# Optimization experiments

Hardware: AMD Instinct MI355X
Metric: run time of the kernel (lower is better)

Reference implementation:

```python
import jax, jax.numpy as jnp
from jax import lax
import numpy as np

B, C, O, NF, H, W = 4, 64, 64, 64, 128, 128
DK = 3
K = DK * DK
PAD = DK // 2


def setup_inputs() -> dict:
    key = jax.random.key(0)
    k0, k1, k2, k3 = jax.random.split(key, 4)
    inputs = jax.random.normal(k0, (B, C, H, W), jnp.float32)
    feat = jax.random.normal(k1, (B, NF, H, W), jnp.float32)
    # small offset-conv weights keep learned offsets in a realistic sub-pixel range
    om_w = jax.random.normal(k2, (C * 3 * K, NF, 3, 3), jnp.float32) * 0.02
    om_b = jnp.zeros((C * 3 * K,), jnp.float32)
    dc_w = jax.random.normal(k3, (O, C, DK, DK), jnp.float32) * (1.0 / np.sqrt(C * K))
    dc_b = jnp.zeros((O,), jnp.float32)
    return dict(inputs=inputs, feat=feat, om_w=om_w, om_b=om_b, dc_w=dc_w, dc_b=dc_b)


def _gather(img, y, x):
    # img: [B,C,H,W]; y,x: int32 [B,C,K,H,W]; zero outside bounds
    valid = (y >= 0) & (y < H) & (x >= 0) & (x < W)
    yc = jnp.clip(y, 0, H - 1)
    xc = jnp.clip(x, 0, W - 1)
    idx = (yc * W + xc).reshape(B, C, K, H * W)
    flat = img.reshape(B, C, 1, H * W)
    v = jnp.take_along_axis(flat, idx, axis=3).reshape(B, C, K, H, W)
    return jnp.where(valid, v, 0.0)


def _forward(inputs, feat, om_w, om_b, dc_w, dc_b):
    # offset/mask conv: nf -> in_nc*3*K, 3x3, pad 1
    off_msk = lax.conv_general_dilated(
        feat, om_w, (1, 1), ((1, 1), (1, 1)),
        dimension_numbers=('NCHW', 'OIHW', 'NCHW')) + om_b[None, :, None, None]
    # offsets interleaved (y,x) per kernel tap per deformable group (= channel)
    off = off_msk[:, :C * 2 * K].reshape(B, C, K, 2, H, W)
    msk = jax.nn.sigmoid(off_msk[:, C * 2 * K:]).reshape(B, C, K, H, W)

    ky = (jnp.arange(K) // DK - PAD).astype(jnp.float32)  # [K]
    kx = (jnp.arange(K) % DK - PAD).astype(jnp.float32)
    hg = jnp.arange(H, dtype=jnp.float32)
    wg = jnp.arange(W, dtype=jnp.float32)
    py = hg[None, None, None, :, None] + ky[None, None, :, None, None] + off[:, :, :, 0]  # [B,C,K,H,W]
    px = wg[None, None, None, None, :] + kx[None, None, :, None, None] + off[:, :, :, 1]

    y0f = jnp.floor(py); x0f = jnp.floor(px)
    wy = py - y0f; wx = px - x0f
    y0 = y0f.astype(jnp.int32); x0 = x0f.astype(jnp.int32)
    y1 = y0 + 1; x1 = x0 + 1

    v00 = _gather(inputs, y0, x0)
    v01 = _gather(inputs, y0, x1)
    v10 = _gather(inputs, y1, x0)
    v11 = _gather(inputs, y1, x1)
    sampled = ((1 - wy) * (1 - wx) * v00 + (1 - wy) * wx * v01
               + wy * (1 - wx) * v10 + wy * wx * v11) * msk  # [B,C,K,H,W]

    out = jnp.einsum('bckhw,ock->bohw', sampled, dc_w.reshape(O, C, K))
    out = out + dc_b[None, :, None, None]
    return jax.nn.relu(out)


def reference(inputs, feat, om_w, om_b, dc_w, dc_b):
    return _forward(inputs, feat, om_w, om_b, dc_w, dc_b)
```

## Files before the change

kernel.cpp:

```cpp
#include <hip/hip_runtime.h>
#include <hip/hip_bf16.h>

typedef __bf16 bf16;
typedef __bf16 bf16x8 __attribute__((ext_vector_type(8)));
typedef __bf16 bf16x4 __attribute__((ext_vector_type(4)));
typedef float f32x4 __attribute__((ext_vector_type(4)));

#define MFMA16(a, b, c) __builtin_amdgcn_mfma_f32_16x16x32_bf16((a), (b), (c), 0, 0, 0)

static constexpr size_t FEAT_OFF = 0;
static constexpr size_t OMW3_OFF = 8388608;
static constexpr size_t OMB_OFF  = OMW3_OFF + 1990656;
static constexpr size_t DCW_OFF  = OMB_OFF + 6912;
static constexpr size_t PAD_OFF  = DCW_OFF + 73728;

__global__ void prep_cvt(const float* __restrict__ in, bf16* __restrict__ out, int n) {
    int i = blockIdx.x * 256 + threadIdx.x;
    if (i < n) out[i] = (bf16)in[i];
}

__global__ void prep_omw3(const float* __restrict__ om_w, bf16* __restrict__ out) {
    int i = blockIdx.x * 256 + threadIdx.x;
    if (i >= 995328) return;
    int e = i & 511, lane = e >> 3, j = e & 7;
    int q = i >> 9;
    int t = q % 3, q2 = q / 3, kk = q2 % 18, ct = q2 / 18;
    int ck = ct * 16 + (lane & 15);
    int kcol = kk * 32 + (lane >> 4) * 8 + j;
    int tap = kcol >> 6, cf = kcol & 63;
    int ch = (t < 2) ? (ck * 2 + t) : (1152 + ck);
    out[i] = (bf16)om_w[ch * 576 + cf * 9 + tap];
}

__global__ void prep_dcw2p(const float* __restrict__ dc_w, const float* __restrict__ om_b,
                           bf16* __restrict__ dcw2p, float* __restrict__ ombr) {
    int i = blockIdx.x * 256 + threadIdx.x;
    if (i < 36864) {
        int j = i & 7, lane = (i >> 3) & 63, ot = (i >> 9) & 3, win = i >> 11;
        int o = ot * 16 + (lane & 15);
        int ck = win * 32 + (lane >> 4) * 8 + j;
        dcw2p[i] = (bf16)dc_w[o * 576 + ck];
    }
    if (i < 1728) {
        int t = i / 576, ck = i - t * 576;
        int ch = (t < 2) ? (ck * 2 + t) : (1152 + ck);
        ombr[i] = om_b[ch];
    }
}

__global__ void prep_pad(const float* __restrict__ inputs, float* __restrict__ pad) {
    int yy = blockIdx.x, bc = blockIdx.y, xx = threadIdx.x;
    if (xx >= 134) return;
    float v = 0.f;
    if (yy >= 3 && yy <= 130 && xx >= 3 && xx <= 130)
        v = inputs[(size_t)bc * 16384 + (yy - 3) * 128 + (xx - 3)];
    pad[((size_t)bc * 134 + yy) * 134 + xx] = v;
}


__global__ void __launch_bounds__(256) __attribute__((amdgpu_waves_per_eu(2, 2)))
deform_fused(const float* __restrict__ pad,
             const bf16* __restrict__ featbf,
             const bf16* __restrict__ omw3,
             const float* __restrict__ ombr,
             const bf16* __restrict__ dcw2p,
             const float* __restrict__ dcb,
             float* __restrict__ out)
{
    const int bh = blockIdx.x;
    const int b = bh >> 7, h = bh & 127;
    const int tid = threadIdx.x;
    const int lane = tid & 63, wid = tid >> 6;
    const int l15 = lane & 15, g = lane >> 4;
    const int ckh = wid & 1, pxh = wid >> 1;

    __shared__ __align__(16) unsigned char smem[49920 + 16384];
    char* featB = (char*)smem;
    char* sampB = (char*)smem + 49920;

    for (int i = tid; i < 12480; i += 256) ((unsigned*)featB)[i] = 0u;
    __syncthreads();
    if (tid < 192) {
        const int ky = tid >> 6, cf = tid & 63;
        const int hh = h - 1 + ky;
        if ((unsigned)hh < 128u) {
            const bf16* src = featbf + (size_t)((b * 64 + cf) * 128 + hh) * 128;
            const int cfb = cf >> 3, cfl = (cf & 7) << 1;
            for (int c0 = 0; c0 < 128; c0 += 8) {
                bf16x8 v = *(const bf16x8*)(src + c0);
#pragma unroll
                for (int e = 0; e < 8; ++e) {
                    int pc = c0 + e + 1;
                    *(bf16*)(featB + (ky * 130 + pc) * 128 + ((cfb ^ (pc & 7)) << 4) + cfl) = v[e];
                }
            }
        }
    }
    __syncthreads();

    f32x4 acc2[8];
#pragma unroll
    for (int u = 0; u < 8; ++u) acc2[u] = (f32x4){0.f, 0.f, 0.f, 0.f};

    const float* padb = pad + (size_t)b * 64 * 17956 + 405;
    const float fx0 = (float)(pxh * 64 + l15);

#pragma unroll 1
    for (int blk = 0; blk < 9; ++blk) {
        f32x4 acc1[3][2][4];
#pragma unroll
        for (int t = 0; t < 3; ++t)
#pragma unroll
            for (int ct = 0; ct < 2; ++ct)
#pragma unroll
                for (int nf = 0; nf < 4; ++nf) acc1[t][ct][nf] = (f32x4){0.f, 0.f, 0.f, 0.f};

        const int ct0 = blk * 4 + ckh * 2;

#pragma unroll 2
        for (int kk = 0; kk < 18; ++kk) {
            const int tap = kk >> 1;
            const int kyp = tap / 3, kxp = tap - 3 * kyp;
            const int pcb = pxh * 64 + l15 + kxp;
            const int base = (kyp * 130 + pcb) * 128 + ((((kk & 1) * 4 + g) ^ (pcb & 7)) << 4);
            bf16x8 a0[3], a1[3];
#pragma unroll
            for (int t = 0; t < 3; ++t) {
                a0[t] = *(const bf16x8*)(omw3 + (size_t)(((ct0 * 18 + kk) * 3 + t) * 512) + lane * 8);
                a1[t] = *(const bf16x8*)(omw3 + (size_t)((((ct0 + 1) * 18 + kk) * 3 + t) * 512) + lane * 8);
            }
#pragma unroll
            for (int nf = 0; nf < 4; ++nf) {
                bf16x8 bfr = *(const bf16x8*)(featB + base + nf * 2048);
                acc1[0][0][nf] = MFMA16(a0[0], bfr, acc1[0][0][nf]);
                acc1[1][0][nf] = MFMA16(a0[1], bfr, acc1[1][0][nf]);
                acc1[2][0][nf] = MFMA16(a0[2], bfr, acc1[2][0][nf]);
                acc1[0][1][nf] = MFMA16(a1[0], bfr, acc1[0][1][nf]);
                acc1[1][1][nf] = MFMA16(a1[1], bfr, acc1[1][1][nf]);
                acc1[2][1][nf] = MFMA16(a1[2], bfr, acc1[2][1][nf]);
            }
        }

        bf16x8 aK0 = *(const bf16x8*)(dcw2p + (size_t)(((blk * 2 + 0) * 4 + wid) * 512) + lane * 8);
        bf16x8 aK1 = *(const bf16x8*)(dcw2p + (size_t)(((blk * 2 + 1) * 4 + wid) * 512) + lane * 8);

#pragma unroll
        for (int ct = 0; ct < 2; ++ct) {
            const float* pl[4];
            float bye[4], bxe[4], bm[4];
#pragma unroll
            for (int r = 0; r < 4; ++r) {
                int ck = blk * 64 + ckh * 32 + ct * 16 + g * 4 + r;
                int c = ck / 9, kd = ck - 9 * c, kq = kd / 3;
                pl[r] = padb + (size_t)c * 17956;
                bye[r] = ombr[ck] + (float)(h + kq - 1);
                bxe[r] = ombr[576 + ck] + (float)(kd - 3 * kq - 1);
                bm[r]  = ombr[1152 + ck];
            }
#pragma unroll
            for (int nf = 0; nf < 4; ++nf) {
                const float fxn = fx0 + 16.f * (float)nf;
                float s[4];
#pragma unroll
                for (int r = 0; r < 4; ++r) {
                    float py = acc1[0][ct][nf][r] + bye[r];
                    float px = acc1[1][ct][nf][r] + bxe[r] + fxn;
                    float lg = acc1[2][ct][nf][r] + bm[r];
                    py = fminf(fmaxf(py, -2.5f), 129.5f);
                    px = fminf(fmaxf(px, -2.5f), 129.5f);
                    float y0f = floorf(py), x0f = floorf(px);
                    float wy = py - y0f, wx = px - x0f;
                    int idx = (int)y0f * 134 + (int)x0f;
                    const float* p0 = pl[r] + idx;
                    float v00 = p0[0], v01 = p0[1], v10 = p0[134], v11 = p0[135];
                    float top = v00 + wx * (v01 - v00);
                    float bot = v10 + wx * (v11 - v10);
                    float bil = top + wy * (bot - top);
                    float msk = __builtin_amdgcn_rcpf(1.f + __expf(-lg));
                    s[r] = bil * msk;
                }
                bf16x4 p = {(bf16)s[0], (bf16)s[1], (bf16)s[2], (bf16)s[3]};
                *(bf16x4*)(sampB + (pxh * 64 + nf * 16 + l15) * 128
                           + (((ckh * 8 + ct * 4 + g) ^ ((l15 & 7) << 1)) << 3)) = p;
            }
        }
        __syncthreads();

#pragma unroll
        for (int u = 0; u < 8; ++u) {
            const int rb = (u * 16 + l15) * 128;
            bf16x8 b0 = *(const bf16x8*)(sampB + rb + ((g ^ (l15 & 7)) << 4));
            bf16x8 b1 = *(const bf16x8*)(sampB + rb + (((4 + g) ^ (l15 & 7)) << 4));
            acc2[u] = MFMA16(aK0, b0, acc2[u]);
            acc2[u] = MFMA16(aK1, b1, acc2[u]);
        }
        __syncthreads();
    }

    float bias[4];
#pragma unroll
    for (int r = 0; r < 4; ++r) bias[r] = dcb[wid * 16 + g * 4 + r];
#pragma unroll
    for (int u = 0; u < 8; ++u)
#pragma unroll
        for (int r = 0; r < 4; ++r) {
            int o = wid * 16 + g * 4 + r;
            out[((size_t)(b * 64 + o) * 128 + h) * 128 + u * 16 + l15]
                = fmaxf(acc2[u][r] + bias[r], 0.f);
        }
}

extern "C" void kernel_launch(void* const* d_in, const int* in_sizes, int n_in,
                              void* d_out, int out_size, void* d_ws, size_t ws_size,
                              hipStream_t stream) {
    const float* inputs = (const float*)d_in[0];
    const float* feat   = (const float*)d_in[1];
    const float* om_w   = (const float*)d_in[2];
    const float* om_b   = (const float*)d_in[3];
    const float* dc_w   = (const float*)d_in[4];
    const float* dc_b   = (const float*)d_in[5];
    float* out = (float*)d_out;

    char* ws = (char*)d_ws;
    bf16*  featbf = (bf16*)(ws + FEAT_OFF);
    bf16*  omw3   = (bf16*)(ws + OMW3_OFF);
    float* ombr   = (float*)(ws + OMB_OFF);
    bf16*  dcw2p  = (bf16*)(ws + DCW_OFF);
    float* pad    = (float*)(ws + PAD_OFF);

    prep_cvt<<<(4194304 + 255) / 256, 256, 0, stream>>>(feat, featbf, 4194304);
    prep_omw3<<<(995328 + 255) / 256, 256, 0, stream>>>(om_w, omw3);
    prep_dcw2p<<<(36864 + 255) / 256, 256, 0, stream>>>(dc_w, om_b, dcw2p, ombr);
    prep_pad<<<dim3(134, 256), 256, 0, stream>>>(inputs, pad);

    deform_fused<<<512, 256, 0, stream>>>(pad, featbf, omw3, ombr, dcw2p, dc_b, out);
}
```

Measured before the change: 181.2 us.

## Split rows into half-width blocks and pre-swizzle feature map in prep kernel

Each block now handles 64 pixels of a row instead of 128, doubling the grid to 1024 blocks and halving shared memory and accumulator registers so more blocks can be resident. Each wave now owns one 16-channel tile of the offset conv instead of splitting channel pairs by pixel half. The feature map is transposed and swizzled into a channel-last bf16 layout by a new prep kernel, so the main kernel loads it with 16-byte copies instead of scalar scattered stores. It also adds s_setprio around MFMA bursts and simplifies the bilinear index math using an offset-by-3 coordinate. The cost is that the omw3 weights are reloaded by twice as many blocks and the halo columns are duplicated between the two blocks of a row.

```diff
diff --git a/kernel.cpp b/kernel.cpp
--- a/kernel.cpp
+++ b/kernel.cpp
@@ -5,18 +5,37 @@
 typedef __bf16 bf16x8 __attribute__((ext_vector_type(8)));
 typedef __bf16 bf16x4 __attribute__((ext_vector_type(4)));
 typedef float f32x4 __attribute__((ext_vector_type(4)));
+typedef int i32x4 __attribute__((ext_vector_type(4)));
 
 #define MFMA16(a, b, c) __builtin_amdgcn_mfma_f32_16x16x32_bf16((a), (b), (c), 0, 0, 0)
 
-static constexpr size_t FEAT_OFF = 0;
-static constexpr size_t OMW3_OFF = 8388608;
-static constexpr size_t OMB_OFF  = OMW3_OFF + 1990656;
-static constexpr size_t DCW_OFF  = OMB_OFF + 6912;
-static constexpr size_t PAD_OFF  = DCW_OFF + 73728;
-
-__global__ void prep_cvt(const float* __restrict__ in, bf16* __restrict__ out, int n) {
-    int i = blockIdx.x * 256 + threadIdx.x;
-    if (i < n) out[i] = (bf16)in[i];
+static constexpr size_t FEATS_OFF = 0;
+static constexpr size_t OMW3_OFF  = 8388608;
+static constexpr size_t OMB_OFF   = OMW3_OFF + 1990656;
+static constexpr size_t DCW_OFF   = OMB_OFF + 6912;
+static constexpr size_t PAD_OFF   = DCW_OFF + 73728;
+
+
+__global__ void prep_featS(const float* __restrict__ feat, bf16* __restrict__ featS) {
+    const int hh = blockIdx.x, b = blockIdx.y;
+    __shared__ float t[64][129];
+    for (int i = threadIdx.x; i < 64 * 32; i += 256) {
+        int cf = i >> 5, q = i & 31;
+        const float* src = feat + ((size_t)(b * 64 + cf) * 128 + hh) * 128 + q * 4;
+        t[cf][q * 4 + 0] = src[0];
+        t[cf][q * 4 + 1] = src[1];
+        t[cf][q * 4 + 2] = src[2];
+        t[cf][q * 4 + 3] = src[3];
+    }
+    __syncthreads();
+    for (int i = threadIdx.x; i < 1024; i += 256) {
+        int px = i >> 3, cfb = i & 7;
+        int sb = cfb ^ (px & 7);
+        bf16x8 v;
+#pragma unroll
+        for (int e = 0; e < 8; ++e) v[e] = (bf16)t[cfb * 8 + e][px];
+        *(bf16x8*)(featS + ((size_t)((b * 128 + hh) * 128 + px) << 6) + sb * 8) = v;
+    }
 }
 
 __global__ void prep_omw3(const float* __restrict__ om_w, bf16* __restrict__ out) {
@@ -58,104 +77,98 @@
 }
 
 
-__global__ void __launch_bounds__(256) __attribute__((amdgpu_waves_per_eu(2, 2)))
+__global__ void __launch_bounds__(256, 4)
 deform_fused(const float* __restrict__ pad,
-             const bf16* __restrict__ featbf,
+             const bf16* __restrict__ featS,
              const bf16* __restrict__ omw3,
              const float* __restrict__ ombr,
              const bf16* __restrict__ dcw2p,
              const float* __restrict__ dcb,
              float* __restrict__ out)
 {
-    const int bh = blockIdx.x;
-    const int b = bh >> 7, h = bh & 127;
+    const int bid = blockIdx.x;
+    const int P0 = (bid & 1) << 6;
+    const int h = (bid >> 1) & 127;
+    const int b = bid >> 8;
     const int tid = threadIdx.x;
     const int lane = tid & 63, wid = tid >> 6;
     const int l15 = lane & 15, g = lane >> 4;
-    const int ckh = wid & 1, pxh = wid >> 1;
-
-    __shared__ __align__(16) unsigned char smem[49920 + 16384];
+
+    __shared__ __align__(16) unsigned char smem[25344 + 8192];
     char* featB = (char*)smem;
-    char* sampB = (char*)smem + 49920;
-
-    for (int i = tid; i < 12480; i += 256) ((unsigned*)featB)[i] = 0u;
+    char* sampB = (char*)smem + 25344;
+
+    for (int i = tid; i < 6336; i += 256) ((unsigned*)featB)[i] = 0u;
     __syncthreads();
-    if (tid < 192) {
-        const int ky = tid >> 6, cf = tid & 63;
-        const int hh = h - 1 + ky;
-        if ((unsigned)hh < 128u) {
-            const bf16* src = featbf + (size_t)((b * 64 + cf) * 128 + hh) * 128;
-            const int cfb = cf >> 3, cfl = (cf & 7) << 1;
-            for (int c0 = 0; c0 < 128; c0 += 8) {
-                bf16x8 v = *(const bf16x8*)(src + c0);
-#pragma unroll
-                for (int e = 0; e < 8; ++e) {
-                    int pc = c0 + e + 1;
-                    *(bf16*)(featB + (ky * 130 + pc) * 128 + ((cfb ^ (pc & 7)) << 4) + cfl) = v[e];
-                }
+    {
+        const int s0 = (P0 == 0) ? 0 : 63;
+        const int q0 = (P0 == 0) ? 1 : 0;
+        for (int i = tid; i < 1560; i += 256) {
+            int ky = i / 520, rem = i - ky * 520, row = rem >> 3, c = rem & 7;
+            int hh = h - 1 + ky;
+            if ((unsigned)hh < 128u) {
+                const char* src = (const char*)featS
+                    + (((size_t)(b * 128 + hh) * 128 + s0 + row) << 7) + c * 16;
+                *(i32x4*)(featB + ((ky * 66 + q0 + row) << 7) + c * 16) = *(const i32x4*)src;
             }
         }
     }
     __syncthreads();
 
-    f32x4 acc2[8];
-#pragma unroll
-    for (int u = 0; u < 8; ++u) acc2[u] = (f32x4){0.f, 0.f, 0.f, 0.f};
-
-    const float* padb = pad + (size_t)b * 64 * 17956 + 405;
-    const float fx0 = (float)(pxh * 64 + l15);
+    f32x4 acc2[4];
+#pragma unroll
+    for (int u = 0; u < 4; ++u) acc2[u] = (f32x4){0.f, 0.f, 0.f, 0.f};
+
+    const float* padb0 = pad + (size_t)b * 64 * 17956;
+    const float fx0 = (float)(P0 + l15);
 
 #pragma unroll 1
     for (int blk = 0; blk < 9; ++blk) {
-        f32x4 acc1[3][2][4];
+        f32x4 acc1[3][4];
 #pragma unroll
         for (int t = 0; t < 3; ++t)
 #pragma unroll
-            for (int ct = 0; ct < 2; ++ct)
-#pragma unroll
-                for (int nf = 0; nf < 4; ++nf) acc1[t][ct][nf] = (f32x4){0.f, 0.f, 0.f, 0.f};
-
-        const int ct0 = blk * 4 + ckh * 2;
+            for (int nf = 0; nf < 4; ++nf) acc1[t][nf] = (f32x4){0.f, 0.f, 0.f, 0.f};
+
+        const int ct = blk * 4 + wid;
 
 #pragma unroll 2
         for (int kk = 0; kk < 18; ++kk) {
             const int tap = kk >> 1;
             const int kyp = tap / 3, kxp = tap - 3 * kyp;
-            const int pcb = pxh * 64 + l15 + kxp;
-            const int base = (kyp * 130 + pcb) * 128 + ((((kk & 1) * 4 + g) ^ (pcb & 7)) << 4);
-            bf16x8 a0[3], a1[3];
-#pragma unroll
-            for (int t = 0; t < 3; ++t) {
-                a0[t] = *(const bf16x8*)(omw3 + (size_t)(((ct0 * 18 + kk) * 3 + t) * 512) + lane * 8);
-                a1[t] = *(const bf16x8*)(omw3 + (size_t)((((ct0 + 1) * 18 + kk) * 3 + t) * 512) + lane * 8);
-            }
+            bf16x8 a0 = *(const bf16x8*)(omw3 + (size_t)(((ct * 18 + kk) * 3 + 0) * 512) + lane * 8);
+            bf16x8 a1 = *(const bf16x8*)(omw3 + (size_t)(((ct * 18 + kk) * 3 + 1) * 512) + lane * 8);
+            bf16x8 a2 = *(const bf16x8*)(omw3 + (size_t)(((ct * 18 + kk) * 3 + 2) * 512) + lane * 8);
+            const int q = l15 + kxp;
+            const int base = (kyp * 66 + q) * 128 + ((((kk & 1) * 4 + g) ^ ((q + 7) & 7)) << 4);
+            bf16x8 bfr[4];
+#pragma unroll
+            for (int nf = 0; nf < 4; ++nf)
+                bfr[nf] = *(const bf16x8*)(featB + base + nf * 2048);
+            __builtin_amdgcn_s_setprio(1);
 #pragma unroll
             for (int nf = 0; nf < 4; ++nf) {
-                bf16x8 bfr = *(const bf16x8*)(featB + base + nf * 2048);
-                acc1[0][0][nf] = MFMA16(a0[0], bfr, acc1[0][0][nf]);
-                acc1[1][0][nf] = MFMA16(a0[1], bfr, acc1[1][0][nf]);
-                acc1[2][0][nf] = MFMA16(a0[2], bfr, acc1[2][0][nf]);
-                acc1[0][1][nf] = MFMA16(a1[0], bfr, acc1[0][1][nf]);
-                acc1[1][1][nf] = MFMA16(a1[1], bfr, acc1[1][1][nf]);
-                acc1[2][1][nf] = MFMA16(a1[2], bfr, acc1[2][1][nf]);
-            }
+                acc1[0][nf] = MFMA16(a0, bfr[nf], acc1[0][nf]);
+                acc1[1][nf] = MFMA16(a1, bfr[nf], acc1[1][nf]);
+                acc1[2][nf] = MFMA16(a2, bfr[nf], acc1[2][nf]);
+            }
+            __builtin_amdgcn_s_setprio(0);
         }
 
         bf16x8 aK0 = *(const bf16x8*)(dcw2p + (size_t)(((blk * 2 + 0) * 4 + wid) * 512) + lane * 8);
         bf16x8 aK1 = *(const bf16x8*)(dcw2p + (size_t)(((blk * 2 + 1) * 4 + wid) * 512) + lane * 8);
 
-#pragma unroll
-        for (int ct = 0; ct < 2; ++ct) {
-            const float* pl[4];
-            float bye[4], bxe[4], bm[4];
+        {
+            unsigned coff[4];
+            float bye3[4], bxe3[4], bm[4];
 #pragma unroll
             for (int r = 0; r < 4; ++r) {
-                int ck = blk * 64 + ckh * 32 + ct * 16 + g * 4 + r;
+                int ck = blk * 64 + wid * 16 + g * 4 + r;
                 int c = ck / 9, kd = ck - 9 * c, kq = kd / 3;
-                pl[r] = padb + (size_t)c * 17956;
-                bye[r] = ombr[ck] + (float)(h + kq - 1);
-                bxe[r] = ombr[576 + ck] + (float)(kd - 3 * kq - 1);
-                bm[r]  = ombr[1152 + ck];
+                coff[r] = (unsigned)(c * 17956);
+                bye3[r] = ombr[ck] + (float)(h + kq + 2);
+                bxe3[r] = ombr[576 + ck] + (float)(kd - 3 * kq + 2);
+                bm[r]   = ombr[1152 + ck];
             }
 #pragma unroll
             for (int nf = 0; nf < 4; ++nf) {
@@ -163,37 +176,39 @@
                 float s[4];
 #pragma unroll
                 for (int r = 0; r < 4; ++r) {
-                    float py = acc1[0][ct][nf][r] + bye[r];
-                    float px = acc1[1][ct][nf][r] + bxe[r] + fxn;
-                    float lg = acc1[2][ct][nf][r] + bm[r];
-                    py = fminf(fmaxf(py, -2.5f), 129.5f);
-                    px = fminf(fmaxf(px, -2.5f), 129.5f);
-                    float y0f = floorf(py), x0f = floorf(px);
-                    float wy = py - y0f, wx = px - x0f;
-                    int idx = (int)y0f * 134 + (int)x0f;
-                    const float* p0 = pl[r] + idx;
-                    float v00 = p0[0], v01 = p0[1], v10 = p0[134], v11 = p0[135];
+                    float py3 = acc1[0][nf][r] + bye3[r];
+                    float px3 = acc1[1][nf][r] + bxe3[r] + fxn;
+                    float lg  = acc1[2][nf][r] + bm[r];
+                    py3 = fminf(fmaxf(py3, 0.5f), 132.5f);
+                    px3 = fminf(fmaxf(px3, 0.5f), 132.5f);
+                    int y03 = (int)py3, x03 = (int)px3;
+                    float wy = py3 - (float)y03, wx = px3 - (float)x03;
+                    unsigned uoff = coff[r] + (unsigned)(y03 * 134 + x03);
+                    const float* p = padb0 + uoff;
+                    float v00 = p[0], v01 = p[1], v10 = p[134], v11 = p[135];
                     float top = v00 + wx * (v01 - v00);
                     float bot = v10 + wx * (v11 - v10);
                     float bil = top + wy * (bot - top);
                     float msk = __builtin_amdgcn_rcpf(1.f + __expf(-lg));
                     s[r] = bil * msk;
                 }
-                bf16x4 p = {(bf16)s[0], (bf16)s[1], (bf16)s[2], (bf16)s[3]};
-                *(bf16x4*)(sampB + (pxh * 64 + nf * 16 + l15) * 128
-                           + (((ckh * 8 + ct * 4 + g) ^ ((l15 & 7) << 1)) << 3)) = p;
+                bf16x4 pk = {(bf16)s[0], (bf16)s[1], (bf16)s[2], (bf16)s[3]};
+                *(bf16x4*)(sampB + (nf * 16 + l15) * 128
+                           + (((wid * 4 + g) ^ ((l15 & 7) << 1)) << 3)) = pk;
             }
         }
         __syncthreads();
 
-#pragma unroll
-        for (int u = 0; u < 8; ++u) {
+        __builtin_amdgcn_s_setprio(1);
+#pragma unroll
+        for (int u = 0; u < 4; ++u) {
             const int rb = (u * 16 + l15) * 128;
             bf16x8 b0 = *(const bf16x8*)(sampB + rb + ((g ^ (l15 & 7)) << 4));
             bf16x8 b1 = *(const bf16x8*)(sampB + rb + (((4 + g) ^ (l15 & 7)) << 4));
             acc2[u] = MFMA16(aK0, b0, acc2[u]);
             acc2[u] = MFMA16(aK1, b1, acc2[u]);
         }
+        __builtin_amdgcn_s_setprio(0);
         __syncthreads();
     }
 
@@ -201,11 +216,11 @@
 #pragma unroll
     for (int r = 0; r < 4; ++r) bias[r] = dcb[wid * 16 + g * 4 + r];
 #pragma unroll
-    for (int u = 0; u < 8; ++u)
+    for (int u = 0; u < 4; ++u)
 #pragma unroll
         for (int r = 0; r < 4; ++r) {
             int o = wid * 16 + g * 4 + r;
-            out[((size_t)(b * 64 + o) * 128 + h) * 128 + u * 16 + l15]
+            out[((size_t)(b * 64 + o) * 128 + h) * 128 + P0 + u * 16 + l15]
                 = fmaxf(acc2[u][r] + bias[r], 0.f);
         }
 }
@@ -222,16 +237,16 @@
     float* out = (float*)d_out;
 
     char* ws = (char*)d_ws;
-    bf16*  featbf = (bf16*)(ws + FEAT_OFF);
+    bf16*  featS  = (bf16*)(ws + FEATS_OFF);
     bf16*  omw3   = (bf16*)(ws + OMW3_OFF);
     float* ombr   = (float*)(ws + OMB_OFF);
     bf16*  dcw2p  = (bf16*)(ws + DCW_OFF);
     float* pad    = (float*)(ws + PAD_OFF);
 
-    prep_cvt<<<(4194304 + 255) / 256, 256, 0, stream>>>(feat, featbf, 4194304);
+    prep_featS<<<dim3(128, 4), 256, 0, stream>>>(feat, featS);
     prep_omw3<<<(995328 + 255) / 256, 256, 0, stream>>>(om_w, omw3);
     prep_dcw2p<<<(36864 + 255) / 256, 256, 0, stream>>>(dc_w, om_b, dcw2p, ombr);
     prep_pad<<<dim3(134, 256), 256, 0, stream>>>(inputs, pad);
 
-    deform_fused<<<512, 256, 0, stream>>>(pad, featbf, omw3, ombr, dcw2p, dc_b, out);
-}
+    deform_fused<<<1024, 256, 0, stream>>>(pad, featS, omw3, ombr, dcw2p, dc_b, out);
+}
```

After: 180.9 us. No clear change (-0.2%).
